# Kernel tuning notes

Hardware: AMD Instinct MI355X
Metric: run time of the kernel (lower is better)

Reference implementation:

```python
import jax, jax.numpy as jnp
import numpy as np

B, N, C, H = 32, 577, 768, 12

def setup_inputs() -> dict:
    key = jax.random.key(0)
    k1, k2, k3, k4 = jax.random.split(key, 4)
    x = jax.random.normal(k1, (B, N, C), dtype=jnp.float32)
    prev = jax.random.normal(k2, (B, H, N, N), dtype=jnp.float32)
    Wqkv = jax.random.normal(k3, (3 * C, C), dtype=jnp.float32) * (C ** -0.5)
    Wproj = jax.random.normal(k4, (C, C), dtype=jnp.float32) * (C ** -0.5)
    bproj = jnp.zeros((C,), dtype=jnp.float32)
    return {"x": x, "prev": prev, "Wqkv": Wqkv, "Wproj": Wproj, "bproj": bproj}

def reference(x, prev, Wqkv, Wproj, bproj):
    b, n, c = x.shape
    h = H
    hd = c // h
    scale = hd ** -0.5
    # qkv: [B, N, 3C] -> [3, B, H, N, hd]
    qkv = (x @ Wqkv.T).reshape(b, n, 3, h, hd).transpose(2, 0, 3, 1, 4)
    q, k, v = qkv[0], qkv[1], qkv[2]
    # pre-softmax scores with residual passthrough (res_score=True)
    scores = jnp.einsum('bhqd,bhkd->bhqk', q, k) * scale + prev
    attn = jax.nn.softmax(scores, axis=-1)
    out = jnp.einsum('bhqk,bhkd->bhqd', attn, v)  # [B, H, N, hd]
    out = out.transpose(0, 2, 1, 3).reshape(b, n, c)
    out = out @ Wproj.T + bproj
    return out, scores
```

## Files before the change

### kernel.cpp

```cpp
#include <hip/hip_runtime.h>
#include <cstdint>
#include <cstddef>

using short8   = __attribute__((ext_vector_type(8))) short;
using f32x4    = __attribute__((ext_vector_type(4))) float;
using ushort4v = __attribute__((ext_vector_type(4))) unsigned short;

#define B_    32
#define N_    577
#define C_    768
#define H_    12
#define HD_   64
#define NPAD  640
#define MROWS 18464
#define MPAD  18560
#define NQKV  2304
#define SCALE 0.125f
#define OUT0_ELTS 14180352

static __device__ __forceinline__ unsigned short f2bf(float f) {
  union { float f; unsigned int u; } v; v.f = f;
  return (unsigned short)((v.u + 0x7FFFu + ((v.u >> 16) & 1u)) >> 16);
}

static __device__ __forceinline__ void gload_lds16(const unsigned short* g, unsigned short* l) {
  __builtin_amdgcn_global_load_lds(
      (const __attribute__((address_space(1))) unsigned int*)g,
      (__attribute__((address_space(3))) unsigned int*)l, 16, 0, 0);
}

__global__ __launch_bounds__(256) void cvt_f32_bf16(const float* __restrict__ src,
                                                    unsigned short* __restrict__ dst, int n4) {
  int i = blockIdx.x * 256 + threadIdx.x;
  if (i >= n4) return;
  f32x4 v = ((const f32x4*)src)[i];
  ushort4v o;
  o.x = f2bf(v.x); o.y = f2bf(v.y); o.z = f2bf(v.z); o.w = f2bf(v.w);
  ((ushort4v*)dst)[i] = o;
}

__global__ __launch_bounds__(256) void gemm_qkv(
    const unsigned short* __restrict__ A,
    const unsigned short* __restrict__ Bw,
    unsigned short* __restrict__ qb,
    unsigned short* __restrict__ kbuf,
    unsigned short* __restrict__ vtb)
{
  __shared__ union {
    struct { unsigned short A[128 * 64]; unsigned short B[128 * 64]; } st;
    unsigned short ct[128 * 128];
  } lds;
  const int mt = blockIdx.x, nt = blockIdx.y;
  const int tid = threadIdx.x;
  const int wave = tid >> 6, lane = tid & 63;
  const int wm = wave >> 1, wn = wave & 1;
  const int lq = lane & 15, grp = lane >> 4;

  f32x4 acc[4][4] = {};

  const int arowbase = mt * 128;
  const int browbase = nt * 128;
  const int srow = wave * 8 + (lane >> 3);
  const int scol = (lane & 7) * 8;

  for (int kblk = 0; kblk < 12; ++kblk) {
    const int koff = kblk * 64;
#pragma unroll
    for (int i = 0; i < 4; ++i) {
      gload_lds16(A  + (size_t)(arowbase + i * 32 + srow) * 768 + koff + scol,
                  &lds.st.A[(i * 32 + wave * 8) * 64]);
      gload_lds16(Bw + (size_t)(browbase + i * 32 + srow) * 768 + koff + scol,
                  &lds.st.B[(i * 32 + wave * 8) * 64]);
    }
    __syncthreads();
#pragma unroll
    for (int ks = 0; ks < 2; ++ks) {
      short8 af[4], bf[4];
#pragma unroll
      for (int mi = 0; mi < 4; ++mi)
        af[mi] = *(const short8*)&lds.st.A[(wm * 64 + mi * 16 + lq) * 64 + ks * 32 + grp * 8];
#pragma unroll
      for (int ni = 0; ni < 4; ++ni)
        bf[ni] = *(const short8*)&lds.st.B[(wn * 64 + ni * 16 + lq) * 64 + ks * 32 + grp * 8];
#pragma unroll
      for (int mi = 0; mi < 4; ++mi)
#pragma unroll
        for (int ni = 0; ni < 4; ++ni)
          acc[mi][ni] = __builtin_amdgcn_mfma_f32_16x16x32_bf16(af[mi], bf[ni], acc[mi][ni], 0, 0, 0);
    }
    __syncthreads();
  }

  const int s = nt / 6;

  if (s < 2) {
#pragma unroll
    for (int mi = 0; mi < 4; ++mi)
#pragma unroll
      for (int ni = 0; ni < 4; ++ni) {
        const int col = wn * 64 + ni * 16 + lq;
#pragma unroll
        for (int j = 0; j < 4; ++j) {
          const int row = wm * 64 + mi * 16 + grp * 4 + j;
          const int slot = (col >> 3) ^ (row & 7);
          lds.ct[row * 128 + slot * 8 + (col & 7)] = f2bf(acc[mi][ni][j]);
        }
      }
    __syncthreads();
    unsigned short* dstbase = (s == 0) ? qb : kbuf;
    const int h0 = (nt - s * 6) * 2;
#pragma unroll
    for (int p = 0; p < 4; ++p) {
      const int r  = p * 32 + (tid >> 3);
      const int cp = tid & 7;
      const int m  = arowbase + r;
      const unsigned bb = (unsigned)m / 577u;
      const int t = m - (int)bb * 577;
      const bool valid = (m < MROWS);
#pragma unroll
      for (int hh = 0; hh < 2; ++hh) {
        const int slot = ((hh * 8 + cp) ^ (r & 7));
        short8 val = *(const short8*)&lds.ct[r * 128 + slot * 8];
        if (valid) {
          unsigned short* dst = dstbase +
              (((size_t)(bb * H_ + h0 + hh) * NPAD + t) * HD_ + cp * 8);
          *(short8*)dst = val;
        }
      }
    }
  } else {
#pragma unroll
    for (int mi = 0; mi < 4; ++mi) {
#pragma unroll
      for (int ni = 0; ni < 4; ++ni) {
        const int n = browbase + wn * 64 + ni * 16 + lq;
        const int rem = n - 1536;
        const int hh = rem >> 6, d = rem & 63;
#pragma unroll
        for (int j = 0; j < 4; ++j) {
          const int m = arowbase + wm * 64 + mi * 16 + grp * 4 + j;
          if (m < MROWS) {
            const unsigned bb = (unsigned)m / 577u;
            const int t = m - (int)bb * 577;
            vtb[((size_t)bb * H_ + hh) * HD_ * NPAD + (size_t)d * NPAD + t] =
                f2bf(acc[mi][ni][j]);
          }
        }
      }
    }
  }
}

__global__ __launch_bounds__(256, 3) void attn_kernel(
    const unsigned short* __restrict__ qb,
    const unsigned short* __restrict__ kb,
    const unsigned short* __restrict__ vtb,
    const float* __restrict__ prev,
    float* __restrict__ scores_out,
    unsigned short* __restrict__ ob)
{
  const int qblk = blockIdx.x;
  const int bh   = blockIdx.y;
  const int tid  = threadIdx.x;
  const int wave = tid >> 6;
  const int lane = tid & 63;
  const int lq = lane & 15, grp = lane >> 4;

  const int b = bh / H_;
  const int h = bh - b * H_;

  const unsigned short* qp = qb  + (size_t)bh * NPAD * HD_;
  const unsigned short* kp = kb  + (size_t)bh * NPAD * HD_;
  const unsigned short* vp = vtb + (size_t)bh * HD_ * NPAD;

  const int qrow = qblk * 64 + wave * 16 + lq;
  const bool qvalid = (qrow < N_);

  const float* prevrow_c = prev + ((size_t)bh * N_ + (qvalid ? qrow : (N_ - 1))) * N_;
  float* srow_base = scores_out + (size_t)bh * N_ * N_;

  __shared__ __attribute__((aligned(16))) unsigned short ldsK[2][4096];
  __shared__ __attribute__((aligned(16))) unsigned short ldsV[2][4096];
  __shared__ __attribute__((aligned(16))) float sslab[4][16][68];

  short8 qf0, qf1;
  {
    const unsigned short* qr = qp + (size_t)qrow * HD_ + grp * 8;
    qf0 = *(const short8*)(qr);
    qf1 = *(const short8*)(qr + 32);
  }

  f32x4 oacc[4] = {};
  float lacc = 0.f;

  const int rhi = tid >> 3;
  const int chk = (tid & 7) ^ (rhi & 7);
  auto stageKV = [&](int kblk, int bufi) {
    const int kbase = kblk * 64;
#pragma unroll
    for (int r = 0; r < 2; ++r) {
      gload_lds16(kp + (size_t)(kbase + r * 32 + rhi) * HD_ + chk * 8,
                  &ldsK[bufi][r * 2048 + wave * 512]);
      gload_lds16(vp + (size_t)(r * 32 + rhi) * NPAD + kbase + chk * 8,
                  &ldsV[bufi][r * 2048 + wave * 512]);
    }
  };

  auto loadPrev = [&](int kblk, float pv[16]) {
#pragma unroll
    for (int t = 0; t < 4; ++t) {
      const int kg0 = kblk * 64 + t * 16 + grp * 4;
      float tmp[4] = {0.f, 0.f, 0.f, 0.f};
      if (kg0 + 3 < N_) {
        __builtin_memcpy(tmp, prevrow_c + kg0, 16);
      } else {
#pragma unroll
        for (int e = 0; e < 4; ++e)
          if (kg0 + e < N_) tmp[e] = prevrow_c[kg0 + e];
      }
#pragma unroll
      for (int e = 0; e < 4; ++e) pv[t * 4 + e] = tmp[e];
    }
  };

  const int sl0 = ((grp)     ^ (lq & 7)) * 8;
  const int sl1 = ((grp + 4) ^ (lq & 7)) * 8;

  float pv[16], pvn[16];
  stageKV(0, 0);
  asm volatile("" ::: "memory");
  loadPrev(0, pv);
  asm volatile("" ::: "memory");
  asm volatile("s_waitcnt vmcnt(4)" ::: "memory");
  __builtin_amdgcn_s_barrier();
  __builtin_amdgcn_sched_barrier(0);

#pragma unroll 1
  for (int kblk = 0; kblk < 10; ++kblk) {
    const int cur = kblk & 1;
    const int kbase = kblk * 64;

    if (kblk < 9) {
      stageKV(kblk + 1, cur ^ 1);
      asm volatile("" ::: "memory");
      loadPrev(kblk + 1, pvn);
      asm volatile("" ::: "memory");
    }

    f32x4 sacc[4] = {};
#pragma unroll
    for (int t = 0; t < 4; ++t) {
      const int row = (t * 16 + lq) * 64;
      short8 a0 = *(const short8*)&ldsK[cur][row + sl0];
      short8 a1 = *(const short8*)&ldsK[cur][row + sl1];
      sacc[t] = __builtin_amdgcn_mfma_f32_16x16x32_bf16(a0, qf0, sacc[t], 0, 0, 0);
      sacc[t] = __builtin_amdgcn_mfma_f32_16x16x32_bf16(a1, qf1, sacc[t], 0, 0, 0);
    }

#pragma unroll
    for (int t = 0; t < 4; ++t) {
      const int kg0 = kbase + t * 16 + grp * 4;
      f32x4 sv;
#pragma unroll
      for (int r = 0; r < 4; ++r) {
        float sval = sacc[t][r] * SCALE + pv[t * 4 + r];
        if (kg0 + r >= N_) sval = -__builtin_inff();
        sv[r] = sval;
      }
      *(f32x4*)&sslab[wave][lq][t * 16 + grp * 4] = sv;
    }

    short8 pf0, pf1;
    {
      const float* sr = &sslab[wave][lq][0];
      f32x4 x0 = *(const f32x4*)(sr + grp * 8);
      f32x4 x1 = *(const f32x4*)(sr + grp * 8 + 4);
      f32x4 x2 = *(const f32x4*)(sr + 32 + grp * 8);
      f32x4 x3 = *(const f32x4*)(sr + 32 + grp * 8 + 4);
      float e[16];
#pragma unroll
      for (int j = 0; j < 4; ++j) {
        e[j]      = __expf(x0[j]);
        e[4 + j]  = __expf(x1[j]);
        e[8 + j]  = __expf(x2[j]);
        e[12 + j] = __expf(x3[j]);
      }
#pragma unroll
      for (int j = 0; j < 16; ++j) lacc += e[j];
      ushort4v pa, pb2, pc, pd;
#pragma unroll
      for (int j = 0; j < 4; ++j) {
        ((unsigned short*)&pa)[j]  = f2bf(e[j]);
        ((unsigned short*)&pb2)[j] = f2bf(e[4 + j]);
        ((unsigned short*)&pc)[j]  = f2bf(e[8 + j]);
        ((unsigned short*)&pd)[j]  = f2bf(e[12 + j]);
      }
      union { struct { ushort4v a, b; } s; short8 v; } u0, u1;
      u0.s.a = pa; u0.s.b = pb2; pf0 = u0.v;
      u1.s.a = pc; u1.s.b = pd;  pf1 = u1.v;
    }

#pragma unroll
    for (int dt = 0; dt < 4; ++dt) {
      const int row = (dt * 16 + lq) * 64;
      short8 v0 = *(const short8*)&ldsV[cur][row + sl0];
      short8 v1 = *(const short8*)&ldsV[cur][row + sl1];
      oacc[dt] = __builtin_amdgcn_mfma_f32_16x16x32_bf16(v0, pf0, oacc[dt], 0, 0, 0);
      oacc[dt] = __builtin_amdgcn_mfma_f32_16x16x32_bf16(v1, pf1, oacc[dt], 0, 0, 0);
    }

#pragma unroll
    for (int q4 = 0; q4 < 4; ++q4) {
      const int row16 = q4 * 4 + (lane >> 4);
      const int qrow_s = qblk * 64 + wave * 16 + row16;
      const int col0 = (lane & 15) * 4;
      const int kg = kbase + col0;
      if (qrow_s < N_) {
        f32x4 vals = *(const f32x4*)&sslab[wave][row16][col0];
        float* dst = srow_base + (size_t)qrow_s * N_ + kg;
        if (kg + 3 < N_) {
          __builtin_memcpy(dst, &vals, 16);
        } else {
#pragma unroll
          for (int e2 = 0; e2 < 4; ++e2)
            if (kg + e2 < N_) dst[e2] = vals[e2];
        }
      }
    }

    if (kblk < 9) {
      if (kblk == 8) asm volatile("s_waitcnt vmcnt(0)" ::: "memory");
      else           asm volatile("s_waitcnt vmcnt(4)" ::: "memory");
      __builtin_amdgcn_s_barrier();
      __builtin_amdgcn_sched_barrier(0);
#pragma unroll
      for (int i = 0; i < 16; ++i) pv[i] = pvn[i];
    }
  }

  lacc += __shfl_xor(lacc, 16, 64);
  lacc += __shfl_xor(lacc, 32, 64);

  if (qvalid) {
    const float rl = 1.0f / lacc;
    unsigned short* orow = ob + (size_t)(b * N_ + qrow) * C_ + h * HD_;
#pragma unroll
    for (int dt = 0; dt < 4; ++dt) {
      ushort4v ow;
      ow.x = f2bf(oacc[dt][0] * rl); ow.y = f2bf(oacc[dt][1] * rl);
      ow.z = f2bf(oacc[dt][2] * rl); ow.w = f2bf(oacc[dt][3] * rl);
      *(ushort4v*)(orow + dt * 16 + grp * 4) = ow;
    }
  }
}

__global__ __launch_bounds__(256) void gemm_proj(
    const unsigned short* __restrict__ A,
    const unsigned short* __restrict__ Bw,
    const float* __restrict__ bias,
    float* __restrict__ out0)
{
  __shared__ unsigned short As[128 * 64];
  __shared__ unsigned short Bs[128 * 64];
  const int mt = blockIdx.x, nt = blockIdx.y;
  const int tid = threadIdx.x;
  const int wave = tid >> 6, lane = tid & 63;
  const int wm = wave >> 1, wn = wave & 1;
  const int lq = lane & 15, grp = lane >> 4;

  f32x4 acc[4][4] = {};

  const int arowbase = mt * 128;
  const int browbase = nt * 128;
  const int srow = wave * 8 + (lane >> 3);
  const int scol = (lane & 7) * 8;

  for (int kblk = 0; kblk < 12; ++kblk) {
    const int koff = kblk * 64;
#pragma unroll
    for (int i = 0; i < 4; ++i) {
      gload_lds16(A  + (size_t)(arowbase + i * 32 + srow) * 768 + koff + scol,
                  &As[(i * 32 + wave * 8) * 64]);
      gload_lds16(Bw + (size_t)(browbase + i * 32 + srow) * 768 + koff + scol,
                  &Bs[(i * 32 + wave * 8) * 64]);
    }
    __syncthreads();
#pragma unroll
    for (int ks = 0; ks < 2; ++ks) {
      short8 af[4], bf[4];
#pragma unroll
      for (int mi = 0; mi < 4; ++mi)
        af[mi] = *(const short8*)&As[(wm * 64 + mi * 16 + lq) * 64 + ks * 32 + grp * 8];
#pragma unroll
      for (int ni = 0; ni < 4; ++ni)
        bf[ni] = *(const short8*)&Bs[(wn * 64 + ni * 16 + lq) * 64 + ks * 32 + grp * 8];
#pragma unroll
      for (int mi = 0; mi < 4; ++mi)
#pragma unroll
        for (int ni = 0; ni < 4; ++ni)
          acc[mi][ni] = __builtin_amdgcn_mfma_f32_16x16x32_bf16(af[mi], bf[ni], acc[mi][ni], 0, 0, 0);
    }
    __syncthreads();
  }

#pragma unroll
  for (int ni = 0; ni < 4; ++ni) {
    const int n = browbase + wn * 64 + ni * 16 + lq;
    const float bv = bias[n];
#pragma unroll
    for (int mi = 0; mi < 4; ++mi) {
#pragma unroll
      for (int j = 0; j < 4; ++j) {
        const int m = arowbase + wm * 64 + mi * 16 + grp * 4 + j;
        if (m < MROWS) out0[(size_t)m * C_ + n] = acc[mi][ni][j] + bv;
      }
    }
  }
}

extern "C" void kernel_launch(void* const* d_in, const int* in_sizes, int n_in,
                              void* d_out, int out_size, void* d_ws, size_t ws_size,
                              hipStream_t stream) {
  const float* x     = (const float*)d_in[0];
  const float* prev  = (const float*)d_in[1];
  const float* Wqkv  = (const float*)d_in[2];
  const float* Wproj = (const float*)d_in[3];
  const float* bproj = (const float*)d_in[4];
  float* out = (float*)d_out;

  char* ws = (char*)d_ws;
  size_t off = 0;
  auto alloc = [&](size_t bytes) {
    void* p = ws + off;
    off += (bytes + 255) & ~(size_t)255;
    return p;
  };
  unsigned short* xb     = (unsigned short*)alloc((size_t)MPAD * 768 * 2);
  unsigned short* wqkvb  = (unsigned short*)alloc((size_t)NQKV * 768 * 2);
  unsigned short* wprojb = (unsigned short*)alloc((size_t)768 * 768 * 2);
  unsigned short* qb     = (unsigned short*)alloc((size_t)B_ * H_ * NPAD * HD_ * 2);
  unsigned short* kbuf   = (unsigned short*)alloc((size_t)B_ * H_ * NPAD * HD_ * 2);
  unsigned short* vtb    = (unsigned short*)alloc((size_t)B_ * H_ * HD_ * NPAD * 2);
  unsigned short* ob     = (unsigned short*)alloc((size_t)MPAD * 768 * 2);
  (void)ob;

  hipMemsetAsync(vtb, 0, (size_t)B_ * H_ * HD_ * NPAD * 2, stream);

  {
    int n4 = (B_ * N_ * C_) / 4;
    cvt_f32_bf16<<<(n4 + 255) / 256, 256, 0, stream>>>(x, xb, n4);
    n4 = (NQKV * C_) / 4;
    cvt_f32_bf16<<<(n4 + 255) / 256, 256, 0, stream>>>(Wqkv, wqkvb, n4);
    n4 = (C_ * C_) / 4;
    cvt_f32_bf16<<<(n4 + 255) / 256, 256, 0, stream>>>(Wproj, wprojb, n4);
  }

  gemm_qkv<<<dim3(MPAD / 128, NQKV / 128), 256, 0, stream>>>(xb, wqkvb, qb, kbuf, vtb);

  attn_kernel<<<dim3(10, B_ * H_), 256, 0, stream>>>(qb, kbuf, vtb, prev,
                                                     out + OUT0_ELTS, ob);

  gemm_proj<<<dim3(MPAD / 128, C_ / 128), 256, 0, stream>>>(ob, wprojb, bproj, out);
}
```

Before: 597.9 us.

## Pre-swizzle Q/K/V layouts in GEMM epilogue and peel tail key block

The QKV GEMM epilogue now writes Q, K and transposed V with the XOR swizzle already applied, so the attention kernel can stage tiles into LDS with plain contiguous addresses. The attention loop runs nine full 64-key blocks with no bounds checks or masking on prev loads and score stores. The single leftover key (index 576) is handled in a separate peeled step with one MFMA pair. This removes per-element masking and branching from the hot loop, at the cost of a more complex wait-count schedule and a hard dependence on N=577.

```diff
diff --git a/kernel.cpp b/kernel.cpp
--- a/kernel.cpp
+++ b/kernel.cpp
@@ -117,13 +117,14 @@
       const unsigned bb = (unsigned)m / 577u;
       const int t = m - (int)bb * 577;
       const bool valid = (m < MROWS);
+      const int cpos = cp ^ (t & 7);
 #pragma unroll
       for (int hh = 0; hh < 2; ++hh) {
         const int slot = ((hh * 8 + cp) ^ (r & 7));
         short8 val = *(const short8*)&lds.ct[r * 128 + slot * 8];
         if (valid) {
           unsigned short* dst = dstbase +
-              (((size_t)(bb * H_ + h0 + hh) * NPAD + t) * HD_ + cp * 8);
+              (((size_t)(bb * H_ + h0 + hh) * NPAD + t) * HD_ + cpos * 8);
           *(short8*)dst = val;
         }
       }
@@ -142,7 +143,9 @@
           if (m < MROWS) {
             const unsigned bb = (unsigned)m / 577u;
             const int t = m - (int)bb * 577;
-            vtb[((size_t)bb * H_ + hh) * HD_ * NPAD + (size_t)d * NPAD + t] =
+            const int tloc = t & 63;
+            const int newcol = (t & ~63) + ((((tloc >> 3) ^ (d & 7)) << 3)) + (t & 7);
+            vtb[((size_t)bb * H_ + hh) * HD_ * NPAD + (size_t)d * NPAD + newcol] =
                 f2bf(acc[mi][ni][j]);
           }
         }
@@ -185,23 +188,23 @@
 
   short8 qf0, qf1;
   {
-    const unsigned short* qr = qp + (size_t)qrow * HD_ + grp * 8;
-    qf0 = *(const short8*)(qr);
-    qf1 = *(const short8*)(qr + 32);
+    const unsigned short* qr = qp + (size_t)qrow * HD_;
+    qf0 = *(const short8*)(qr + ((grp)     ^ (lq & 7)) * 8);
+    qf1 = *(const short8*)(qr + ((grp + 4) ^ (lq & 7)) * 8);
   }
 
   f32x4 oacc[4] = {};
   float lacc = 0.f;
 
-  const int rhi = tid >> 3;
-  const int chk = (tid & 7) ^ (rhi & 7);
+  const int srow8 = wave * 8 + (lane >> 3);
+  const int scol8 = (lane & 7) * 8;
   auto stageKV = [&](int kblk, int bufi) {
     const int kbase = kblk * 64;
 #pragma unroll
     for (int r = 0; r < 2; ++r) {
-      gload_lds16(kp + (size_t)(kbase + r * 32 + rhi) * HD_ + chk * 8,
+      gload_lds16(kp + (size_t)(kbase + r * 32 + srow8) * HD_ + scol8,
                   &ldsK[bufi][r * 2048 + wave * 512]);
-      gload_lds16(vp + (size_t)(r * 32 + rhi) * NPAD + kbase + chk * 8,
+      gload_lds16(vp + (size_t)(r * 32 + srow8) * NPAD + kbase + scol8,
                   &ldsV[bufi][r * 2048 + wave * 512]);
     }
   };
@@ -210,14 +213,8 @@
 #pragma unroll
     for (int t = 0; t < 4; ++t) {
       const int kg0 = kblk * 64 + t * 16 + grp * 4;
-      float tmp[4] = {0.f, 0.f, 0.f, 0.f};
-      if (kg0 + 3 < N_) {
-        __builtin_memcpy(tmp, prevrow_c + kg0, 16);
-      } else {
-#pragma unroll
-        for (int e = 0; e < 4; ++e)
-          if (kg0 + e < N_) tmp[e] = prevrow_c[kg0 + e];
-      }
+      float tmp[4];
+      __builtin_memcpy(tmp, prevrow_c + kg0, 16);
 #pragma unroll
       for (int e = 0; e < 4; ++e) pv[t * 4 + e] = tmp[e];
     }
@@ -236,16 +233,14 @@
   __builtin_amdgcn_sched_barrier(0);
 
 #pragma unroll 1
-  for (int kblk = 0; kblk < 10; ++kblk) {
+  for (int kblk = 0; kblk < 9; ++kblk) {
     const int cur = kblk & 1;
     const int kbase = kblk * 64;
 
-    if (kblk < 9) {
-      stageKV(kblk + 1, cur ^ 1);
-      asm volatile("" ::: "memory");
-      loadPrev(kblk + 1, pvn);
-      asm volatile("" ::: "memory");
-    }
+    stageKV(kblk + 1, cur ^ 1);
+    asm volatile("" ::: "memory");
+    if (kblk < 8) loadPrev(kblk + 1, pvn);
+    asm volatile("" ::: "memory");
 
     f32x4 sacc[4] = {};
 #pragma unroll
@@ -259,14 +254,10 @@
 
 #pragma unroll
     for (int t = 0; t < 4; ++t) {
-      const int kg0 = kbase + t * 16 + grp * 4;
       f32x4 sv;
 #pragma unroll
-      for (int r = 0; r < 4; ++r) {
-        float sval = sacc[t][r] * SCALE + pv[t * 4 + r];
-        if (kg0 + r >= N_) sval = -__builtin_inff();
-        sv[r] = sval;
-      }
+      for (int r = 0; r < 4; ++r)
+        sv[r] = sacc[t][r] * SCALE + pv[t * 4 + r];
       *(f32x4*)&sslab[wave][lq][t * 16 + grp * 4] = sv;
     }
 
@@ -314,28 +305,42 @@
       const int row16 = q4 * 4 + (lane >> 4);
       const int qrow_s = qblk * 64 + wave * 16 + row16;
       const int col0 = (lane & 15) * 4;
-      const int kg = kbase + col0;
       if (qrow_s < N_) {
         f32x4 vals = *(const f32x4*)&sslab[wave][row16][col0];
-        float* dst = srow_base + (size_t)qrow_s * N_ + kg;
-        if (kg + 3 < N_) {
-          __builtin_memcpy(dst, &vals, 16);
-        } else {
-#pragma unroll
-          for (int e2 = 0; e2 < 4; ++e2)
-            if (kg + e2 < N_) dst[e2] = vals[e2];
-        }
-      }
-    }
-
-    if (kblk < 9) {
-      if (kblk == 8) asm volatile("s_waitcnt vmcnt(0)" ::: "memory");
-      else           asm volatile("s_waitcnt vmcnt(4)" ::: "memory");
-      __builtin_amdgcn_s_barrier();
-      __builtin_amdgcn_sched_barrier(0);
-#pragma unroll
-      for (int i = 0; i < 16; ++i) pv[i] = pvn[i];
-    }
+        __builtin_memcpy(srow_base + (size_t)qrow_s * N_ + kbase + col0, &vals, 16);
+      }
+    }
+
+    if (kblk == 8) asm volatile("s_waitcnt vmcnt(4)" ::: "memory");
+    else           asm volatile("s_waitcnt vmcnt(8)" ::: "memory");
+    __builtin_amdgcn_s_barrier();
+    __builtin_amdgcn_sched_barrier(0);
+#pragma unroll
+    for (int i = 0; i < 16; ++i) pv[i] = pvn[i];
+  }
+
+  {
+    f32x4 s0 = {};
+    {
+      const int row = lq * 64;
+      short8 a0 = *(const short8*)&ldsK[1][row + sl0];
+      short8 a1 = *(const short8*)&ldsK[1][row + sl1];
+      s0 = __builtin_amdgcn_mfma_f32_16x16x32_bf16(a0, qf0, s0, 0, 0, 0);
+      s0 = __builtin_amdgcn_mfma_f32_16x16x32_bf16(a1, qf1, s0, 0, 0, 0);
+    }
+    const float sval9 = s0[0] * SCALE + prevrow_c[576];
+    const float e9 = (grp == 0) ? __expf(sval9) : 0.f;
+    lacc += e9;
+    short8 pf0 = {};
+    ((unsigned short*)&pf0)[0] = f2bf(e9);
+#pragma unroll
+    for (int dt = 0; dt < 4; ++dt) {
+      const int row = (dt * 16 + lq) * 64;
+      short8 v0 = *(const short8*)&ldsV[1][row + sl0];
+      oacc[dt] = __builtin_amdgcn_mfma_f32_16x16x32_bf16(v0, pf0, oacc[dt], 0, 0, 0);
+    }
+    if (grp == 0 && qvalid)
+      srow_base[(size_t)qrow * N_ + 576] = sval9;
   }
 
   lacc += __shfl_xor(lacc, 16, 64);
```

Result: no change. 588.0 us (-1.7%).
